# Kernel optimization log

Measured on AMD Instinct MI355X. Metric: run time of the kernel, lower is better.

The kernel has to match this reference:

```python
import jax, jax.numpy as jnp
import numpy as np

N, B, FIN, E, EDIM, H, C = 20000, 2, 256, 320000, 64, 8, 32


def setup_inputs() -> dict:
    key = jax.random.key(0)
    ks = jax.random.split(key, 12)
    s = 1.0 / np.sqrt(FIN)
    se = 1.0 / np.sqrt(EDIM)
    return {
        "x": jax.random.normal(ks[0], (N, B, FIN), jnp.float32),
        "edata": jax.random.normal(ks[1], (E, EDIM), jnp.float32),
        "edge_src": jax.random.randint(ks[2], (E,), 0, N, jnp.int32),
        "edge_dst": jax.random.randint(ks[3], (E,), 0, N, jnp.int32),
        "Wq": jax.random.normal(ks[4], (FIN, H * C), jnp.float32) * s,
        "bq": jnp.zeros((H * C,), jnp.float32),
        "Wk": jax.random.normal(ks[5], (FIN, H * C), jnp.float32) * s,
        "bk": jnp.zeros((H * C,), jnp.float32),
        "Wv": jax.random.normal(ks[6], (FIN, H * C), jnp.float32) * s,
        "bv": jnp.zeros((H * C,), jnp.float32),
        "We": jax.random.normal(ks[7], (EDIM, H * C), jnp.float32) * se,
        "Wr": jax.random.normal(ks[8], (FIN, H * C), jnp.float32) * s,
        "br": jnp.zeros((H * C,), jnp.float32),
    }


def reference(x, edata, edge_src, edge_dst, Wq, bq, Wk, bk, Wv, bv, We, Wr, br):
    # x: [N, B, FIN]; edata: [E, EDIM]
    q = (x @ Wq + bq).reshape(N, B, H, C)   # dst queries
    k = (x @ Wk + bk).reshape(N, B, H, C)   # src keys
    v = (x @ Wv + bv).reshape(N, B, H, C)   # src values
    e = (edata @ We).reshape(E, 1, H, C)    # edge feats, broadcast over batch

    scale = 1.0 / np.sqrt(C)
    # per-edge logits: (u_mul_v / sqrt(C) + edata).sum(-1) -> [E, B, H]
    logits = (k[edge_src] * q[edge_dst] * scale + e).sum(-1)

    # edge_softmax over edges sharing the same destination node
    m = jax.ops.segment_max(logits, edge_dst, num_segments=N)      # [N, B, H]
    ex = jnp.exp(logits - m[edge_dst])
    z = jax.ops.segment_sum(ex, edge_dst, num_segments=N)          # [N, B, H]
    alpha = ex / z[edge_dst]                                       # [E, B, H]

    # weighted scatter-sum aggregation: u_mul_e + sum over dst
    att_v = v[edge_src] * alpha[..., None]                         # [E, B, H, C]
    agg = jax.ops.segment_sum(att_v, edge_dst, num_segments=N)     # [N, B, H, C]

    out = agg.reshape(N, B, H * C) + (x @ Wr + br)
    return out
```

## Files before the change

### kernel.cpp

```cpp
#include <hip/hip_runtime.h>
#include <hip/hip_bf16.h>

#define NN    20000
#define BB    2
#define EE    320000
#define MROWS (NN * BB)

typedef __bf16 bf16x8 __attribute__((ext_vector_type(8)));
typedef float  floatx4 __attribute__((ext_vector_type(4)));


__global__ __launch_bounds__(256) void transpose_weights(
    const float* __restrict__ Wq, const float* __restrict__ Wk,
    const float* __restrict__ Wv, const float* __restrict__ Wr,
    __hip_bfloat16* __restrict__ wt) {
  __shared__ float TA[32][65];
  __shared__ float TB[32][65];
  int bt = blockIdx.x;
  const float *A, *B;
  int c0, jbase;
  if (bt < 8) { A = Wk; B = Wv; c0 = 32 * bt;      jbase = 64 * bt; }
  else        { A = Wq; B = Wr; c0 = 32 * (bt-8);  jbase = 512 + 64 * (bt-8); }
  int t = threadIdx.x;
  int krow = t >> 2;
  int cc = (t & 3) * 8;
  int sel = t >> 7;
  int u = t & 127;
  int ci = u >> 2;
  int kk0 = (u & 3) * 16;

  for (int kt = 0; kt < 4; ++kt) {
    int k = kt * 64 + krow;
    float4 a0 = *(const float4*)(A + (size_t)k * 256 + c0 + cc);
    float4 a1 = *(const float4*)(A + (size_t)k * 256 + c0 + cc + 4);
    float4 b0 = *(const float4*)(B + (size_t)k * 256 + c0 + cc);
    float4 b1 = *(const float4*)(B + (size_t)k * 256 + c0 + cc + 4);
    __syncthreads();
    TA[cc+0][krow]=a0.x; TA[cc+1][krow]=a0.y; TA[cc+2][krow]=a0.z; TA[cc+3][krow]=a0.w;
    TA[cc+4][krow]=a1.x; TA[cc+5][krow]=a1.y; TA[cc+6][krow]=a1.z; TA[cc+7][krow]=a1.w;
    TB[cc+0][krow]=b0.x; TB[cc+1][krow]=b0.y; TB[cc+2][krow]=b0.z; TB[cc+3][krow]=b0.w;
    TB[cc+4][krow]=b1.x; TB[cc+5][krow]=b1.y; TB[cc+6][krow]=b1.z; TB[cc+7][krow]=b1.w;
    __syncthreads();
    float (*T)[65] = sel ? TB : TA;
    int j = jbase + 2 * ci + sel;
    __hip_bfloat16* dst = wt + (size_t)j * 256 + kt * 64 + kk0;
    #pragma unroll
    for (int q = 0; q < 16; ++q) dst[q] = __float2bfloat16(T[ci][kk0 + q]);
  }
}

__global__ void prep_bias(const float* __restrict__ bq, const float* __restrict__ bk,
                          const float* __restrict__ bv, const float* __restrict__ br,
                          float* __restrict__ bcat) {
  int j = blockIdx.x * 256 + threadIdx.x;
  float val;
  if (j < 512) { int c = j >> 1;         val = (j & 1) ? bv[c] : bk[c]; }
  else         { int c = (j - 512) >> 1; val = (j & 1) ? br[c] : bq[c]; }
  bcat[j] = val;
}

__global__ void prep_wesum(const float* __restrict__ We, float* __restrict__ wesum) {
  int i = threadIdx.x;
  int h = i >> 6, d = i & 63;
  float s = 0.f;
  for (int c = 0; c < 32; ++c) s += We[(size_t)d * 256 + h * 32 + c];
  wesum[h * 64 + d] = s;
}

__global__ void zero_ints(int* __restrict__ p, int n) {
  int i = blockIdx.x * 256 + threadIdx.x;
  if (i < n) p[i] = 0;
}

__global__ __launch_bounds__(256) void gemm_qkvr(
    const float* __restrict__ x,
    const __bf16* __restrict__ wt,
    const float* __restrict__ bcat,
    __hip_bfloat16* __restrict__ out) {
  const int LSTR = 40;
  __shared__ __attribute__((aligned(16))) __bf16 As[64 * LSTR];
  __shared__ __attribute__((aligned(16))) __bf16 Bs[256 * LSTR];

  int m0 = blockIdx.y * 64;
  int n0 = blockIdx.x * 256;
  int t = threadIdx.x;
  int w = t >> 6, l = t & 63;
  int lr = l & 15, lq = l >> 4;
  int ar = t >> 2, ac = (t & 3) * 8;

  floatx4 acc[4][4] = {};

  for (int ks = 0; ks < 8; ++ks) {
    const float* xp = x + (size_t)(m0 + ar) * 256 + ks * 32 + ac;
    float4 f0 = *(const float4*)xp;
    float4 f1 = *(const float4*)(xp + 4);
    bf16x8 av;
    av[0] = (__bf16)f0.x; av[1] = (__bf16)f0.y;
    av[2] = (__bf16)f0.z; av[3] = (__bf16)f0.w;
    av[4] = (__bf16)f1.x; av[5] = (__bf16)f1.y;
    av[6] = (__bf16)f1.z; av[7] = (__bf16)f1.w;
    const __bf16* wp = wt + (size_t)(n0 + t) * 256 + ks * 32;
    bf16x8 b0 = *(const bf16x8*)(wp);
    bf16x8 b1 = *(const bf16x8*)(wp + 8);
    bf16x8 b2 = *(const bf16x8*)(wp + 16);
    bf16x8 b3 = *(const bf16x8*)(wp + 24);
    __syncthreads();
    *(bf16x8*)&As[ar * LSTR + ac] = av;
    __bf16* bsr = &Bs[t * LSTR];
    *(bf16x8*)(bsr)      = b0;
    *(bf16x8*)(bsr + 8)  = b1;
    *(bf16x8*)(bsr + 16) = b2;
    *(bf16x8*)(bsr + 24) = b3;
    __syncthreads();
    bf16x8 af[4], bf_[4];
    #pragma unroll
    for (int mt = 0; mt < 4; ++mt)
      af[mt] = *(const bf16x8*)&As[(16 * mt + lr) * LSTR + lq * 8];
    #pragma unroll
    for (int nt = 0; nt < 4; ++nt)
      bf_[nt] = *(const bf16x8*)&Bs[(64 * w + 16 * nt + lr) * LSTR + lq * 8];
    #pragma unroll
    for (int mt = 0; mt < 4; ++mt)
      #pragma unroll
      for (int nt = 0; nt < 4; ++nt)
        acc[mt][nt] = __builtin_amdgcn_mfma_f32_16x16x32_bf16(af[mt], bf_[nt], acc[mt][nt], 0, 0, 0);
  }

  #pragma unroll
  for (int mt = 0; mt < 4; ++mt)
    #pragma unroll
    for (int nt = 0; nt < 4; ++nt)
      #pragma unroll
      for (int r = 0; r < 4; ++r) {
        int gr = m0 + 16 * mt + lq * 4 + r;
        int gc = n0 + 64 * w + 16 * nt + lr;
        out[(size_t)gr * 1024 + gc] = __float2bfloat16(acc[mt][nt][r] + bcat[gc]);
      }
}

__global__ __launch_bounds__(256) void esum2_kernel(
    const float* __restrict__ edata,
    const float* __restrict__ wesum,
    float* __restrict__ esum) {
  __shared__ float wl[512];
  int t = threadIdx.x;
  wl[t] = wesum[t];
  wl[t + 256] = wesum[t + 256];
  __syncthreads();
  int e = blockIdx.x * 256 + t;
  if (e >= EE) return;
  float acc[8] = {};
  const float* row = edata + (size_t)e * 64;
  for (int d = 0; d < 64; d += 4) {
    float4 v = *(const float4*)(row + d);
    #pragma unroll
    for (int h = 0; h < 8; ++h) {
      const float* wv = &wl[h * 64 + d];
      acc[h] += v.x * wv[0] + v.y * wv[1] + v.z * wv[2] + v.w * wv[3];
    }
  }
  #pragma unroll
  for (int h = 0; h < 8; ++h) esum[(size_t)e * 8 + h] = acc[h];
}

__global__ void hist_kernel(const int* __restrict__ dst, int* __restrict__ counts) {
  int e = blockIdx.x * 256 + threadIdx.x;
  if (e < EE) atomicAdd(&counts[dst[e]], 1);
}

__global__ void scan_kernel(const int* __restrict__ counts,
                            int* __restrict__ offsets,
                            int* __restrict__ cursor) {
  __shared__ int part[256];
  int t = threadIdx.x;
  const int per = (NN + 255) / 256;
  int lo = t * per, hi = min(lo + per, NN);
  int s = 0;
  for (int i = lo; i < hi; ++i) s += counts[i];
  part[t] = s;
  __syncthreads();
  for (int off = 1; off < 256; off <<= 1) {
    int v = (t >= off) ? part[t - off] : 0;
    __syncthreads();
    part[t] += v;
    __syncthreads();
  }
  int base = (t == 0) ? 0 : part[t - 1];
  for (int i = lo; i < hi; ++i) {
    offsets[i] = base;
    cursor[i] = base;
    base += counts[i];
  }
  if (t == 255) offsets[NN] = base;
}

__global__ void scatter_kernel(const int* __restrict__ dst,
                               int* __restrict__ cursor,
                               int* __restrict__ sorted) {
  int e = blockIdx.x * 256 + threadIdx.x;
  if (e < EE) {
    int p = atomicAdd(&cursor[dst[e]], 1);
    sorted[p] = e;
  }
}

__global__ __launch_bounds__(256) void aggregate_kernel(
    const unsigned int* __restrict__ qkvr,
    const float* __restrict__ esum,
    const int* __restrict__ offsets,
    const int* __restrict__ sorted,
    const int* __restrict__ src,
    float* __restrict__ out) {
  int t = threadIdx.x;
  int w = t >> 6, l = t & 63;
  int nb = blockIdx.x * 4 + w;
  int b = nb & 1, n = nb >> 1;
  int h = l >> 3;
  int beg = offsets[n], end = offsets[n + 1];

  uint4 qr4 = *(const uint4*)(qkvr + (size_t)nb * 512 + 256 + l * 4);
  float q0 = __uint_as_float(qr4.x << 16);
  float q1 = __uint_as_float(qr4.y << 16);
  float q2 = __uint_as_float(qr4.z << 16);
  float q3 = __uint_as_float(qr4.w << 16);

  const unsigned* kvbase = qkvr + (size_t)b * 512 + l * 4;
  const float* esbase = esum + h;

  float z = 0.f, a0 = 0.f, a1 = 0.f, a2 = 0.f, a3 = 0.f;

  for (int base = beg; base < end; base += 64) {
    int chunk = min(64, end - base);
    int e_l = 0, s_l = 0;
    if (l < chunk) { e_l = sorted[base + l]; s_l = src[e_l]; }
    uint4 kvA = {0, 0, 0, 0}, kvB = {0, 0, 0, 0};
    float esA = 0.f, esB = 0.f;
    {
      int s0 = __builtin_amdgcn_readlane(s_l, 0);
      int e0 = __builtin_amdgcn_readlane(e_l, 0);
      kvA = *(const uint4*)(kvbase + (size_t)s0 * 1024);
      esA = esbase[(size_t)e0 * 8];
      if (chunk > 1) {
        int s1 = __builtin_amdgcn_readlane(s_l, 1);
        int e1 = __builtin_amdgcn_readlane(e_l, 1);
        kvB = *(const uint4*)(kvbase + (size_t)s1 * 1024);
        esB = esbase[(size_t)e1 * 8];
      }
    }
    for (int i = 0; i < chunk; ++i) {
      uint4 kv = kvA; float es = esA;
      kvA = kvB; esA = esB;
      if (i + 2 < chunk) {
        int s2 = __builtin_amdgcn_readlane(s_l, i + 2);
        int e2 = __builtin_amdgcn_readlane(e_l, i + 2);
        kvB = *(const uint4*)(kvbase + (size_t)s2 * 1024);
        esB = esbase[(size_t)e2 * 8];
      }
      float k0 = __uint_as_float(kv.x << 16);
      float k1 = __uint_as_float(kv.y << 16);
      float k2 = __uint_as_float(kv.z << 16);
      float k3 = __uint_as_float(kv.w << 16);
      float part = k0 * q0 + k1 * q1 + k2 * q2 + k3 * q3;
      part += __shfl_xor(part, 1, 64);
      part += __shfl_xor(part, 2, 64);
      part += __shfl_xor(part, 4, 64);
      float p = __expf(part * 0.17677669529663687f + es);
      z += p;
      float v0 = __uint_as_float(kv.x & 0xFFFF0000u);
      float v1 = __uint_as_float(kv.y & 0xFFFF0000u);
      float v2 = __uint_as_float(kv.z & 0xFFFF0000u);
      float v3 = __uint_as_float(kv.w & 0xFFFF0000u);
      a0 += p * v0; a1 += p * v1; a2 += p * v2; a3 += p * v3;
    }
  }
  float inv = (z > 0.f) ? (1.0f / z) : 0.f;
  float r0 = __uint_as_float(qr4.x & 0xFFFF0000u);
  float r1 = __uint_as_float(qr4.y & 0xFFFF0000u);
  float r2 = __uint_as_float(qr4.z & 0xFFFF0000u);
  float r3 = __uint_as_float(qr4.w & 0xFFFF0000u);
  float4 o = make_float4(a0 * inv + r0, a1 * inv + r1,
                         a2 * inv + r2, a3 * inv + r3);
  *(float4*)(out + (size_t)nb * 256 + l * 4) = o;
}

extern "C" void kernel_launch(void* const* d_in, const int* in_sizes, int n_in,
                              void* d_out, int out_size, void* d_ws, size_t ws_size,
                              hipStream_t stream) {
  (void)in_sizes; (void)n_in; (void)out_size; (void)ws_size;
  const float* x     = (const float*)d_in[0];
  const float* edata = (const float*)d_in[1];
  const int* esrc    = (const int*)d_in[2];
  const int* edst    = (const int*)d_in[3];
  const float* Wq    = (const float*)d_in[4];
  const float* bq    = (const float*)d_in[5];
  const float* Wk    = (const float*)d_in[6];
  const float* bk    = (const float*)d_in[7];
  const float* Wv    = (const float*)d_in[8];
  const float* bv    = (const float*)d_in[9];
  const float* We    = (const float*)d_in[10];
  const float* Wr    = (const float*)d_in[11];
  const float* br    = (const float*)d_in[12];
  float* out = (float*)d_out;

  char* ws = (char*)d_ws;
  size_t off = 0;
  auto carve = [&](size_t bytes) -> void* {
    void* p = ws + off;
    off += (bytes + 255) & ~(size_t)255;
    return p;
  };
  int* counts    = (int*)carve((size_t)NN * 4);
  int* offsets   = (int*)carve((size_t)(NN + 1) * 4);
  int* cursor    = (int*)carve((size_t)NN * 4);
  int* sorted    = (int*)carve((size_t)EE * 4);
  __hip_bfloat16* wt = (__hip_bfloat16*)carve((size_t)1024 * 256 * 2);
  float* bcat    = (float*)carve(1024 * 4);
  float* wesum   = (float*)carve(8 * 64 * 4);
  float* esum    = (float*)carve((size_t)EE * 8 * 4);
  __hip_bfloat16* qkvr = (__hip_bfloat16*)carve((size_t)MROWS * 1024 * 2);

  zero_ints<<<(NN + 255) / 256, 256, 0, stream>>>(counts, NN);
  transpose_weights<<<16, 256, 0, stream>>>(Wq, Wk, Wv, Wr, wt);
  prep_bias<<<4, 256, 0, stream>>>(bq, bk, bv, br, bcat);
  prep_wesum<<<1, 512, 0, stream>>>(We, wesum);
  hist_kernel<<<(EE + 255) / 256, 256, 0, stream>>>(edst, counts);
  scan_kernel<<<1, 256, 0, stream>>>(counts, offsets, cursor);
  scatter_kernel<<<(EE + 255) / 256, 256, 0, stream>>>(edst, cursor, sorted);
  gemm_qkvr<<<dim3(4, 625), 256, 0, stream>>>(x, (const __bf16*)wt, bcat, qkvr);
  esum2_kernel<<<(EE + 255) / 256, 256, 0, stream>>>(edata, wesum, esum);
  aggregate_kernel<<<MROWS / 4, 256, 0, stream>>>((const unsigned int*)qkvr, esum,
                                                  offsets, sorted, esrc, out);
}
```

Baseline: 453.7 us.

## Fuse GEMM with edge-sum, pre-sort edge data, process both batches per wave

The scatter step now writes source indices and each edge's sorted position directly, and the edge-sum kernel writes its results in destination-sorted order. That removes the sorted-id indirection and lets the aggregation read edge scores contiguously. The GEMM and edge-sum are merged into one launch of interleaved block types (two GEMM blocks per edge-sum block) so their different resource demands overlap. The aggregation wave now handles both batch elements of a node, so the edge list and source indices are read once per node instead of once per batch element. The cost is more live registers per wave and a scattered write pattern in the edge-sum.

```diff
diff --git a/kernel.cpp b/kernel.cpp
--- a/kernel.cpp
+++ b/kernel.cpp
@@ -72,97 +72,6 @@
   if (i < n) p[i] = 0;
 }
 
-__global__ __launch_bounds__(256) void gemm_qkvr(
-    const float* __restrict__ x,
-    const __bf16* __restrict__ wt,
-    const float* __restrict__ bcat,
-    __hip_bfloat16* __restrict__ out) {
-  const int LSTR = 40;
-  __shared__ __attribute__((aligned(16))) __bf16 As[64 * LSTR];
-  __shared__ __attribute__((aligned(16))) __bf16 Bs[256 * LSTR];
-
-  int m0 = blockIdx.y * 64;
-  int n0 = blockIdx.x * 256;
-  int t = threadIdx.x;
-  int w = t >> 6, l = t & 63;
-  int lr = l & 15, lq = l >> 4;
-  int ar = t >> 2, ac = (t & 3) * 8;
-
-  floatx4 acc[4][4] = {};
-
-  for (int ks = 0; ks < 8; ++ks) {
-    const float* xp = x + (size_t)(m0 + ar) * 256 + ks * 32 + ac;
-    float4 f0 = *(const float4*)xp;
-    float4 f1 = *(const float4*)(xp + 4);
-    bf16x8 av;
-    av[0] = (__bf16)f0.x; av[1] = (__bf16)f0.y;
-    av[2] = (__bf16)f0.z; av[3] = (__bf16)f0.w;
-    av[4] = (__bf16)f1.x; av[5] = (__bf16)f1.y;
-    av[6] = (__bf16)f1.z; av[7] = (__bf16)f1.w;
-    const __bf16* wp = wt + (size_t)(n0 + t) * 256 + ks * 32;
-    bf16x8 b0 = *(const bf16x8*)(wp);
-    bf16x8 b1 = *(const bf16x8*)(wp + 8);
-    bf16x8 b2 = *(const bf16x8*)(wp + 16);
-    bf16x8 b3 = *(const bf16x8*)(wp + 24);
-    __syncthreads();
-    *(bf16x8*)&As[ar * LSTR + ac] = av;
-    __bf16* bsr = &Bs[t * LSTR];
-    *(bf16x8*)(bsr)      = b0;
-    *(bf16x8*)(bsr + 8)  = b1;
-    *(bf16x8*)(bsr + 16) = b2;
-    *(bf16x8*)(bsr + 24) = b3;
-    __syncthreads();
-    bf16x8 af[4], bf_[4];
-    #pragma unroll
-    for (int mt = 0; mt < 4; ++mt)
-      af[mt] = *(const bf16x8*)&As[(16 * mt + lr) * LSTR + lq * 8];
-    #pragma unroll
-    for (int nt = 0; nt < 4; ++nt)
-      bf_[nt] = *(const bf16x8*)&Bs[(64 * w + 16 * nt + lr) * LSTR + lq * 8];
-    #pragma unroll
-    for (int mt = 0; mt < 4; ++mt)
-      #pragma unroll
-      for (int nt = 0; nt < 4; ++nt)
-        acc[mt][nt] = __builtin_amdgcn_mfma_f32_16x16x32_bf16(af[mt], bf_[nt], acc[mt][nt], 0, 0, 0);
-  }
-
-  #pragma unroll
-  for (int mt = 0; mt < 4; ++mt)
-    #pragma unroll
-    for (int nt = 0; nt < 4; ++nt)
-      #pragma unroll
-      for (int r = 0; r < 4; ++r) {
-        int gr = m0 + 16 * mt + lq * 4 + r;
-        int gc = n0 + 64 * w + 16 * nt + lr;
-        out[(size_t)gr * 1024 + gc] = __float2bfloat16(acc[mt][nt][r] + bcat[gc]);
-      }
-}
-
-__global__ __launch_bounds__(256) void esum2_kernel(
-    const float* __restrict__ edata,
-    const float* __restrict__ wesum,
-    float* __restrict__ esum) {
-  __shared__ float wl[512];
-  int t = threadIdx.x;
-  wl[t] = wesum[t];
-  wl[t + 256] = wesum[t + 256];
-  __syncthreads();
-  int e = blockIdx.x * 256 + t;
-  if (e >= EE) return;
-  float acc[8] = {};
-  const float* row = edata + (size_t)e * 64;
-  for (int d = 0; d < 64; d += 4) {
-    float4 v = *(const float4*)(row + d);
-    #pragma unroll
-    for (int h = 0; h < 8; ++h) {
-      const float* wv = &wl[h * 64 + d];
-      acc[h] += v.x * wv[0] + v.y * wv[1] + v.z * wv[2] + v.w * wv[3];
-    }
-  }
-  #pragma unroll
-  for (int h = 0; h < 8; ++h) esum[(size_t)e * 8 + h] = acc[h];
-}
-
 __global__ void hist_kernel(const int* __restrict__ dst, int* __restrict__ counts) {
   int e = blockIdx.x * 256 + threadIdx.x;
   if (e < EE) atomicAdd(&counts[dst[e]], 1);
@@ -195,12 +104,110 @@
 }
 
 __global__ void scatter_kernel(const int* __restrict__ dst,
+                               const int* __restrict__ src,
                                int* __restrict__ cursor,
-                               int* __restrict__ sorted) {
+                               int* __restrict__ ssrc,
+                               int* __restrict__ pos) {
   int e = blockIdx.x * 256 + threadIdx.x;
   if (e < EE) {
     int p = atomicAdd(&cursor[dst[e]], 1);
-    sorted[p] = e;
+    ssrc[p] = src[e];
+    pos[e] = p;
+  }
+}
+
+__global__ __launch_bounds__(256) void fused_gemm_esum(
+    const float* __restrict__ x,
+    const __bf16* __restrict__ wt,
+    const float* __restrict__ bcat,
+    __hip_bfloat16* __restrict__ outq,
+    const float* __restrict__ edata,
+    const float* __restrict__ wesum,
+    const int* __restrict__ pos,
+    float* __restrict__ esum) {
+  const int LSTR = 40;
+  __shared__ __attribute__((aligned(16))) __bf16 ABs[(64 + 256) * LSTR];
+  int bid = blockIdx.x;
+  int t = threadIdx.x;
+  int g = bid / 3, rsub = bid - g * 3;
+
+  if (rsub < 2) {
+    int gb = g * 2 + rsub;
+    __bf16* As = ABs;
+    __bf16* Bs = ABs + 64 * LSTR;
+    int m0 = (gb >> 2) * 64;
+    int n0 = (gb & 3) * 256;
+    int w = t >> 6, l = t & 63;
+    int lr = l & 15, lq = l >> 4;
+    int ar = t >> 2, ac = (t & 3) * 8;
+
+    floatx4 acc[4][4] = {};
+
+    for (int ks = 0; ks < 8; ++ks) {
+      const float* xp = x + (size_t)(m0 + ar) * 256 + ks * 32 + ac;
+      float4 f0 = *(const float4*)xp;
+      float4 f1 = *(const float4*)(xp + 4);
+      bf16x8 av;
+      av[0] = (__bf16)f0.x; av[1] = (__bf16)f0.y;
+      av[2] = (__bf16)f0.z; av[3] = (__bf16)f0.w;
+      av[4] = (__bf16)f1.x; av[5] = (__bf16)f1.y;
+      av[6] = (__bf16)f1.z; av[7] = (__bf16)f1.w;
+      const __bf16* wp = wt + (size_t)(n0 + t) * 256 + ks * 32;
+      bf16x8 b0 = *(const bf16x8*)(wp);
+      bf16x8 b1 = *(const bf16x8*)(wp + 8);
+      bf16x8 b2 = *(const bf16x8*)(wp + 16);
+      bf16x8 b3 = *(const bf16x8*)(wp + 24);
+      __syncthreads();
+      *(bf16x8*)&As[ar * LSTR + ac] = av;
+      __bf16* bsr = &Bs[t * LSTR];
+      *(bf16x8*)(bsr)      = b0;
+      *(bf16x8*)(bsr + 8)  = b1;
+      *(bf16x8*)(bsr + 16) = b2;
+      *(bf16x8*)(bsr + 24) = b3;
+      __syncthreads();
+      bf16x8 af[4], bf_[4];
+      #pragma unroll
+      for (int mt = 0; mt < 4; ++mt)
+        af[mt] = *(const bf16x8*)&As[(16 * mt + lr) * LSTR + lq * 8];
+      #pragma unroll
+      for (int nt = 0; nt < 4; ++nt)
+        bf_[nt] = *(const bf16x8*)&Bs[(64 * w + 16 * nt + lr) * LSTR + lq * 8];
+      #pragma unroll
+      for (int mt = 0; mt < 4; ++mt)
+        #pragma unroll
+        for (int nt = 0; nt < 4; ++nt)
+          acc[mt][nt] = __builtin_amdgcn_mfma_f32_16x16x32_bf16(af[mt], bf_[nt], acc[mt][nt], 0, 0, 0);
+    }
+
+    #pragma unroll
+    for (int mt = 0; mt < 4; ++mt)
+      #pragma unroll
+      for (int nt = 0; nt < 4; ++nt)
+        #pragma unroll
+        for (int r = 0; r < 4; ++r) {
+          int gr = m0 + 16 * mt + lq * 4 + r;
+          int gc = n0 + 64 * w + 16 * nt + lr;
+          outq[(size_t)gr * 1024 + gc] = __float2bfloat16(acc[mt][nt][r] + bcat[gc]);
+        }
+  } else {
+    float* wl = (float*)ABs;
+    wl[t] = wesum[t];
+    wl[t + 256] = wesum[t + 256];
+    __syncthreads();
+    int e = g * 256 + t;
+    float acc[8] = {};
+    const float* row = edata + (size_t)e * 64;
+    for (int d = 0; d < 64; d += 4) {
+      float4 v = *(const float4*)(row + d);
+      #pragma unroll
+      for (int hh = 0; hh < 8; ++hh) {
+        const float* wv = &wl[hh * 64 + d];
+        acc[hh] += v.x * wv[0] + v.y * wv[1] + v.z * wv[2] + v.w * wv[3];
+      }
+    }
+    float* op = esum + (size_t)pos[e] * 8;
+    *(float4*)op       = make_float4(acc[0], acc[1], acc[2], acc[3]);
+    *(float4*)(op + 4) = make_float4(acc[4], acc[5], acc[6], acc[7]);
   }
 }
 
@@ -208,79 +215,94 @@
     const unsigned int* __restrict__ qkvr,
     const float* __restrict__ esum,
     const int* __restrict__ offsets,
-    const int* __restrict__ sorted,
-    const int* __restrict__ src,
+    const int* __restrict__ ssrc,
     float* __restrict__ out) {
   int t = threadIdx.x;
   int w = t >> 6, l = t & 63;
-  int nb = blockIdx.x * 4 + w;
-  int b = nb & 1, n = nb >> 1;
+  int n = blockIdx.x * 4 + w;
   int h = l >> 3;
   int beg = offsets[n], end = offsets[n + 1];
 
-  uint4 qr4 = *(const uint4*)(qkvr + (size_t)nb * 512 + 256 + l * 4);
-  float q0 = __uint_as_float(qr4.x << 16);
-  float q1 = __uint_as_float(qr4.y << 16);
-  float q2 = __uint_as_float(qr4.z << 16);
-  float q3 = __uint_as_float(qr4.w << 16);
-
-  const unsigned* kvbase = qkvr + (size_t)b * 512 + l * 4;
-  const float* esbase = esum + h;
-
-  float z = 0.f, a0 = 0.f, a1 = 0.f, a2 = 0.f, a3 = 0.f;
+  uint4 qra = *(const uint4*)(qkvr + (size_t)(2 * n) * 512 + 256 + l * 4);
+  uint4 qrb = *(const uint4*)(qkvr + (size_t)(2 * n + 1) * 512 + 256 + l * 4);
+  float qa0 = __uint_as_float(qra.x << 16), qa1 = __uint_as_float(qra.y << 16);
+  float qa2 = __uint_as_float(qra.z << 16), qa3 = __uint_as_float(qra.w << 16);
+  float qb0 = __uint_as_float(qrb.x << 16), qb1 = __uint_as_float(qrb.y << 16);
+  float qb2 = __uint_as_float(qrb.z << 16), qb3 = __uint_as_float(qrb.w << 16);
+
+  const unsigned* kvl = qkvr + l * 4;
+
+  float za = 0.f, zb = 0.f;
+  float aa0 = 0.f, aa1 = 0.f, aa2 = 0.f, aa3 = 0.f;
+  float ab0 = 0.f, ab1 = 0.f, ab2 = 0.f, ab3 = 0.f;
 
   for (int base = beg; base < end; base += 64) {
     int chunk = min(64, end - base);
-    int e_l = 0, s_l = 0;
-    if (l < chunk) { e_l = sorted[base + l]; s_l = src[e_l]; }
-    uint4 kvA = {0, 0, 0, 0}, kvB = {0, 0, 0, 0};
-    float esA = 0.f, esB = 0.f;
+    int s_l = (l < chunk) ? ssrc[base + l] : 0;
+    const float* esp = esum + (size_t)base * 8 + h;
+    uint4 kA0 = {0,0,0,0}, kA1 = {0,0,0,0};
+    uint4 kB0 = {0,0,0,0}, kB1 = {0,0,0,0};
+    float eA = 0.f, eB = 0.f;
     {
       int s0 = __builtin_amdgcn_readlane(s_l, 0);
-      int e0 = __builtin_amdgcn_readlane(e_l, 0);
-      kvA = *(const uint4*)(kvbase + (size_t)s0 * 1024);
-      esA = esbase[(size_t)e0 * 8];
-      if (chunk > 1) {
-        int s1 = __builtin_amdgcn_readlane(s_l, 1);
-        int e1 = __builtin_amdgcn_readlane(e_l, 1);
-        kvB = *(const uint4*)(kvbase + (size_t)s1 * 1024);
-        esB = esbase[(size_t)e1 * 8];
-      }
+      const unsigned* p = kvl + (size_t)s0 * 1024;
+      kA0 = *(const uint4*)p;
+      kA1 = *(const uint4*)(p + 512);
+      eA = esp[0];
+    }
+    if (chunk > 1) {
+      int s1 = __builtin_amdgcn_readlane(s_l, 1);
+      const unsigned* p = kvl + (size_t)s1 * 1024;
+      kB0 = *(const uint4*)p;
+      kB1 = *(const uint4*)(p + 512);
+      eB = esp[8];
     }
     for (int i = 0; i < chunk; ++i) {
-      uint4 kv = kvA; float es = esA;
-      kvA = kvB; esA = esB;
+      uint4 k0 = kA0, k1 = kA1; float es = eA;
+      kA0 = kB0; kA1 = kB1; eA = eB;
       if (i + 2 < chunk) {
         int s2 = __builtin_amdgcn_readlane(s_l, i + 2);
-        int e2 = __builtin_amdgcn_readlane(e_l, i + 2);
-        kvB = *(const uint4*)(kvbase + (size_t)s2 * 1024);
-        esB = esbase[(size_t)e2 * 8];
+        const unsigned* p = kvl + (size_t)s2 * 1024;
+        kB0 = *(const uint4*)p;
+        kB1 = *(const uint4*)(p + 512);
+        eB = esp[(size_t)(i + 2) * 8];
       }
-      float k0 = __uint_as_float(kv.x << 16);
-      float k1 = __uint_as_float(kv.y << 16);
-      float k2 = __uint_as_float(kv.z << 16);
-      float k3 = __uint_as_float(kv.w << 16);
-      float part = k0 * q0 + k1 * q1 + k2 * q2 + k3 * q3;
-      part += __shfl_xor(part, 1, 64);
-      part += __shfl_xor(part, 2, 64);
-      part += __shfl_xor(part, 4, 64);
-      float p = __expf(part * 0.17677669529663687f + es);
-      z += p;
-      float v0 = __uint_as_float(kv.x & 0xFFFF0000u);
-      float v1 = __uint_as_float(kv.y & 0xFFFF0000u);
-      float v2 = __uint_as_float(kv.z & 0xFFFF0000u);
-      float v3 = __uint_as_float(kv.w & 0xFFFF0000u);
-      a0 += p * v0; a1 += p * v1; a2 += p * v2; a3 += p * v3;
-    }
-  }
-  float inv = (z > 0.f) ? (1.0f / z) : 0.f;
-  float r0 = __uint_as_float(qr4.x & 0xFFFF0000u);
-  float r1 = __uint_as_float(qr4.y & 0xFFFF0000u);
-  float r2 = __uint_as_float(qr4.z & 0xFFFF0000u);
-  float r3 = __uint_as_float(qr4.w & 0xFFFF0000u);
-  float4 o = make_float4(a0 * inv + r0, a1 * inv + r1,
-                         a2 * inv + r2, a3 * inv + r3);
-  *(float4*)(out + (size_t)nb * 256 + l * 4) = o;
+      float pa = __uint_as_float(k0.x << 16) * qa0
+               + __uint_as_float(k0.y << 16) * qa1
+               + __uint_as_float(k0.z << 16) * qa2
+               + __uint_as_float(k0.w << 16) * qa3;
+      float pb = __uint_as_float(k1.x << 16) * qb0
+               + __uint_as_float(k1.y << 16) * qb1
+               + __uint_as_float(k1.z << 16) * qb2
+               + __uint_as_float(k1.w << 16) * qb3;
+      pa += __shfl_xor(pa, 1, 64);  pb += __shfl_xor(pb, 1, 64);
+      pa += __shfl_xor(pa, 2, 64);  pb += __shfl_xor(pb, 2, 64);
+      pa += __shfl_xor(pa, 4, 64);  pb += __shfl_xor(pb, 4, 64);
+      float ea_ = __expf(pa * 0.17677669529663687f + es);
+      float eb_ = __expf(pb * 0.17677669529663687f + es);
+      za += ea_; zb += eb_;
+      aa0 += ea_ * __uint_as_float(k0.x & 0xFFFF0000u);
+      aa1 += ea_ * __uint_as_float(k0.y & 0xFFFF0000u);
+      aa2 += ea_ * __uint_as_float(k0.z & 0xFFFF0000u);
+      aa3 += ea_ * __uint_as_float(k0.w & 0xFFFF0000u);
+      ab0 += eb_ * __uint_as_float(k1.x & 0xFFFF0000u);
+      ab1 += eb_ * __uint_as_float(k1.y & 0xFFFF0000u);
+      ab2 += eb_ * __uint_as_float(k1.z & 0xFFFF0000u);
+      ab3 += eb_ * __uint_as_float(k1.w & 0xFFFF0000u);
+    }
+  }
+  float ia = (za > 0.f) ? 1.f / za : 0.f;
+  float ib = (zb > 0.f) ? 1.f / zb : 0.f;
+  float4 oa = make_float4(aa0 * ia + __uint_as_float(qra.x & 0xFFFF0000u),
+                          aa1 * ia + __uint_as_float(qra.y & 0xFFFF0000u),
+                          aa2 * ia + __uint_as_float(qra.z & 0xFFFF0000u),
+                          aa3 * ia + __uint_as_float(qra.w & 0xFFFF0000u));
+  float4 ob = make_float4(ab0 * ib + __uint_as_float(qrb.x & 0xFFFF0000u),
+                          ab1 * ib + __uint_as_float(qrb.y & 0xFFFF0000u),
+                          ab2 * ib + __uint_as_float(qrb.z & 0xFFFF0000u),
+                          ab3 * ib + __uint_as_float(qrb.w & 0xFFFF0000u));
+  *(float4*)(out + (size_t)(2 * n) * 256 + l * 4) = oa;
+  *(float4*)(out + (size_t)(2 * n + 1) * 256 + l * 4) = ob;
 }
 
 extern "C" void kernel_launch(void* const* d_in, const int* in_sizes, int n_in,
@@ -312,7 +334,8 @@
   int* counts    = (int*)carve((size_t)NN * 4);
   int* offsets   = (int*)carve((size_t)(NN + 1) * 4);
   int* cursor    = (int*)carve((size_t)NN * 4);
-  int* sorted    = (int*)carve((size_t)EE * 4);
+  int* ssrc      = (int*)carve((size_t)EE * 4);
+  int* pos       = (int*)carve((size_t)EE * 4);
   __hip_bfloat16* wt = (__hip_bfloat16*)carve((size_t)1024 * 256 * 2);
   float* bcat    = (float*)carve(1024 * 4);
   float* wesum   = (float*)carve(8 * 64 * 4);
@@ -325,9 +348,9 @@
   prep_wesum<<<1, 512, 0, stream>>>(We, wesum);
   hist_kernel<<<(EE + 255) / 256, 256, 0, stream>>>(edst, counts);
   scan_kernel<<<1, 256, 0, stream>>>(counts, offsets, cursor);
-  scatter_kernel<<<(EE + 255) / 256, 256, 0, stream>>>(edst, cursor, sorted);
-  gemm_qkvr<<<dim3(4, 625), 256, 0, stream>>>(x, (const __bf16*)wt, bcat, qkvr);
-  esum2_kernel<<<(EE + 255) / 256, 256, 0, stream>>>(edata, wesum, esum);
-  aggregate_kernel<<<MROWS / 4, 256, 0, stream>>>((const unsigned int*)qkvr, esum,
-                                                  offsets, sorted, esrc, out);
-}
+  scatter_kernel<<<(EE + 255) / 256, 256, 0, stream>>>(edst, esrc, cursor, ssrc, pos);
+  fused_gemm_esum<<<3750, 256, 0, stream>>>(x, (const __bf16*)wt, bcat, qkvr,
+                                            edata, wesum, pos, esum);
+  aggregate_kernel<<<NN / 4, 256, 0, stream>>>((const unsigned int*)qkvr, esum,
+                                               offsets, ssrc, out);
+}
```

Result: no change. 448.5 us (-1.1%).
